# Optimization experiments

Measured on AMD Instinct MI355X. Metric: run time of the kernel, lower is better.

Reference implementation:

```python
import math
import jax, jax.numpy as jnp
import numpy as np

B, T, C, H = 4, 1024, 1024, 16


def setup_inputs() -> dict:
    key = jax.random.key(0)
    k1, k2, k3 = jax.random.split(key, 3)
    scale = 0.02
    return {
        "x": jax.random.normal(k1, (B, T, C), dtype=jnp.float32),
        "w_attn": jax.random.normal(k2, (C, 3 * C), dtype=jnp.float32) * scale,
        "b_attn": jnp.zeros((3 * C,), dtype=jnp.float32),
        "w_proj": jax.random.normal(k3, (C, C), dtype=jnp.float32) * scale,
        "b_proj": jnp.zeros((C,), dtype=jnp.float32),
    }


def reference(x, w_attn, b_attn, w_proj, b_proj):
    b, t, c = x.shape
    h = H
    d = c // h
    qkv = x @ w_attn + b_attn                      # [b, t, 3c]
    q, k, v = jnp.split(qkv, 3, axis=-1)
    # [b, h, t, d]
    q = q.reshape(b, t, h, d).transpose(0, 2, 1, 3)
    k = k.reshape(b, t, h, d).transpose(0, 2, 1, 3)
    v = v.reshape(b, t, h, d).transpose(0, 2, 1, 3)
    att = jnp.einsum("bhqd,bhkd->bhqk", q, k) * (1.0 / math.sqrt(d))
    causal = jnp.tril(jnp.ones((t, t), dtype=bool))
    att = jnp.where(causal[None, None], att, -jnp.inf)
    att = jax.nn.softmax(att, axis=-1)
    # dropout is identity in eval mode
    y = jnp.einsum("bhqk,bhkd->bhqd", att, v)      # [b, h, t, d]
    y = y.transpose(0, 2, 1, 3).reshape(b, t, c)
    return y @ w_proj + b_proj
```

## Files before the change

### kernel.cpp

```cpp
#include <hip/hip_runtime.h>

typedef __bf16 bf16;
typedef float f32x4 __attribute__((ext_vector_type(4)));
typedef bf16 bf16x4 __attribute__((ext_vector_type(4)));
typedef bf16 bf16x8 __attribute__((ext_vector_type(8)));

#define MFMA16(a, b, c) __builtin_amdgcn_mfma_f32_16x16x32_bf16((a), (b), (c), 0, 0, 0)

__device__ __forceinline__ f32x4 zero4() {
    f32x4 z; z[0] = 0.f; z[1] = 0.f; z[2] = 0.f; z[3] = 0.f; return z;
}
__device__ __forceinline__ void gl_lds16(const bf16* g, bf16* l) {
    __builtin_amdgcn_global_load_lds(
        (const __attribute__((address_space(1))) void*)g,
        (__attribute__((address_space(3))) void*)l, 16, 0, 0);
}

__global__ __launch_bounds__(256)
void prep_k(const float* __restrict__ x, bf16* __restrict__ xb,
            const float* __restrict__ w_attn, bf16* __restrict__ wT,
            const float* __restrict__ w_proj, bf16* __restrict__ wpT)
{
    __shared__ bf16 Ls[64][72];
    const int blk = blockIdx.x;
    const int tid = threadIdx.x;

    if (blk < 2048) {
        const int i = (blk * 256 + tid) * 8;
        const float4 a = *(const float4*)(x + i);
        const float4 b = *(const float4*)(x + i + 4);
        bf16x8 o;
        o[0] = (bf16)a.x; o[1] = (bf16)a.y; o[2] = (bf16)a.z; o[3] = (bf16)a.w;
        o[4] = (bf16)b.x; o[5] = (bf16)b.y; o[6] = (bf16)b.z; o[7] = (bf16)b.w;
        *(bf16x8*)(xb + i) = o;
        return;
    }
    const float* src;
    bf16* dst;
    int K, N, bx, by;
    if (blk < 2816) {
        const int r = blk - 2048;
        src = w_attn; dst = wT; K = 1024; N = 3072;
        bx = r % 48; by = r / 48;
    } else {
        const int r = blk - 2816;
        src = w_proj; dst = wpT; K = 1024; N = 1024;
        bx = r & 15; by = r >> 4;
    }
    const int k0 = by << 6;
    const int n0 = bx << 6;
    #pragma unroll
    for (int it = 0; it < 4; ++it) {
        const int lin = (it << 10) + (tid << 2);
        const int r = lin >> 6, c = lin & 63;
        const float4 v = *(const float4*)(src + (size_t)(k0 + r) * N + n0 + c);
        bf16x4 o; o[0] = (bf16)v.x; o[1] = (bf16)v.y; o[2] = (bf16)v.z; o[3] = (bf16)v.w;
        *(bf16x4*)&Ls[r][c] = o;
    }
    __syncthreads();
    #pragma unroll
    for (int it = 0; it < 2; ++it) {
        const int lin = (it << 11) + (tid << 3);
        const int nn = lin >> 6, kk = lin & 63;
        bf16x8 o;
        #pragma unroll
        for (int j = 0; j < 8; ++j) o[j] = Ls[kk + j][nn];
        *(bf16x8*)(dst + (size_t)(n0 + nn) * K + k0 + kk) = o;
    }
}

template <int MODE>
__global__ __launch_bounds__(256)
void gemm_bt(const bf16* __restrict__ A, const bf16* __restrict__ Bt,
             const float* __restrict__ bias,
             bf16* __restrict__ qw, bf16* __restrict__ kw, bf16* __restrict__ vw,
             float* __restrict__ outf, int M, int N, int K)
{
    constexpr int BK = 64;
    constexpr int BN = (MODE == 0) ? 128 : 64;
    constexpr int MF = (MODE == 0) ? 4 : 2;
    constexpr int NF = 4;
    constexpr int BI = (MODE == 0) ? 4 : 2;

    __shared__ __align__(16) bf16 smem[128 * BK + BN * BK];
    bf16* const As = smem;
    bf16* const Bs = smem + 128 * BK;

    const int tid  = threadIdx.x;
    const int lane = tid & 63;
    const int wid  = tid >> 6;
    const int l16  = lane & 15;
    const int g    = lane >> 4;
    const int wrb  = (MODE == 0) ? ((wid >> 1) << 6) : (wid << 5);
    const int wcb  = (MODE == 0) ? ((wid & 1) << 6) : 0;

    const int p   = blockIdx.x;
    const int xcd = p & 7;
    const int r   = p >> 3;
    int by, bx;
    if (MODE == 0) { by = ((xcd >> 1) << 3) + r / 12; bx = (xcd & 1) * 12 + r % 12; }
    else           { by = ((xcd >> 1) << 3) + (r >> 3); bx = ((xcd & 1) << 3) + (r & 7); }
    const int m0 = by << 7;
    const int n0 = bx * BN;

    const int srow = lane >> 3;
    const int sswz = ((lane & 7) ^ srow) << 3;
    const bf16* pa[4];
    const bf16* pb[BI];
    int dA[4], dB[BI];
    #pragma unroll
    for (int i = 0; i < 4; ++i) {
        const int R = (wid << 5) + (i << 3);
        pa[i] = A + (size_t)(m0 + R + srow) * K + sswz;
        dA[i] = R << 6;
    }
    #pragma unroll
    for (int i = 0; i < BI; ++i) {
        const int R = wid * (BN / 4) + (i << 3);
        pb[i] = Bt + (size_t)(n0 + R + srow) * K + sswz;
        dB[i] = R << 6;
    }

    int offA[2][MF], offB[2][NF];
    #pragma unroll
    for (int ks = 0; ks < 2; ++ks) {
        #pragma unroll
        for (int mf = 0; mf < MF; ++mf) {
            const int rr = wrb + (mf << 4) + l16;
            offA[ks][mf] = (rr << 6) + ((((ks << 2) + g) ^ (rr & 7)) << 3);
        }
        #pragma unroll
        for (int nf = 0; nf < NF; ++nf) {
            const int rr = wcb + (nf << 4) + l16;
            offB[ks][nf] = (rr << 6) + ((((ks << 2) + g) ^ (rr & 7)) << 3);
        }
    }

    f32x4 acc[MF][NF];
    #pragma unroll
    for (int i = 0; i < MF; ++i)
        #pragma unroll
        for (int j = 0; j < NF; ++j) acc[i][j] = zero4();

    const int nk = K >> 6;
    for (int kt = 0; kt < nk; ++kt) {
        const int k0 = kt << 6;
        __syncthreads();
        #pragma unroll
        for (int i = 0; i < 4; ++i)  gl_lds16(pa[i] + k0, As + dA[i]);
        #pragma unroll
        for (int i = 0; i < BI; ++i) gl_lds16(pb[i] + k0, Bs + dB[i]);
        __syncthreads();
        #pragma unroll
        for (int ks = 0; ks < 2; ++ks) {
            bf16x8 af[MF], bfr[NF];
            #pragma unroll
            for (int mf = 0; mf < MF; ++mf) af[mf] = *(const bf16x8*)&As[offA[ks][mf]];
            #pragma unroll
            for (int nf = 0; nf < NF; ++nf) bfr[nf] = *(const bf16x8*)&Bs[offB[ks][nf]];
            #pragma unroll
            for (int mf = 0; mf < MF; ++mf)
                #pragma unroll
                for (int nf = 0; nf < NF; ++nf)
                    acc[mf][nf] = MFMA16(af[mf], bfr[nf], acc[mf][nf]);
        }
    }
    __syncthreads();

    if (MODE == 0) {
        bf16* const Es = smem;
        const int bq  = m0 >> 10;
        const int tb  = m0 & 1023;
        const int hh0 = (n0 & 1023) >> 6;
        const bool isV = (n0 >= 2048);
        if (isV) {
            #pragma unroll
            for (int mf = 0; mf < MF; ++mf)
                #pragma unroll
                for (int nf = 0; nf < NF; ++nf) {
                    const int nn = wcb + (nf << 4) + l16;
                    const float bs = bias[n0 + nn];
                    bf16x4 pq;
                    #pragma unroll
                    for (int j = 0; j < 4; ++j) pq[j] = (bf16)(acc[mf][nf][j] + bs);
                    const int m = wrb + (mf << 4) + (g << 2);
                    const int pp = ((m >> 5) << 5) + (((m >> 2) & 3) << 3) + (((m >> 4) & 1) << 2);
                    *(bf16x4*)&Es[nn * 128 + pp] = pq;
                }
        } else {
            #pragma unroll
            for (int mf = 0; mf < MF; ++mf)
                #pragma unroll
                for (int nf = 0; nf < NF; ++nf) {
                    const int nn = wcb + (nf << 4) + l16;
                    const float bs = bias[n0 + nn];
                    #pragma unroll
                    for (int j = 0; j < 4; ++j) {
                        const int mm = wrb + (mf << 4) + (g << 2) + j;
                        Es[mm * 128 + nn] = (bf16)(acc[mf][nf][j] + bs);
                    }
                }
        }
        __syncthreads();
        #pragma unroll
        for (int it = 0; it < 8; ++it) {
            const int idx = (it << 8) + tid;
            const int row = idx >> 4, ch = idx & 15;
            const bf16x8 v = *(const bf16x8*)&Es[row * 128 + (ch << 3)];
            if (isV) {
                const int dd = row & 63, hh = hh0 + (row >> 6);
                *(bf16x8*)(vw + ((size_t)((bq << 4) + hh) << 16) + ((size_t)dd << 10)
                           + tb + (ch << 3)) = v;
            } else {
                const int t = tb + row;
                const int cc = ch << 3;
                const int hh = hh0 + (cc >> 6);
                bf16* const dst = (n0 < 1024) ? qw : kw;
                *(bf16x8*)(dst + ((size_t)((bq << 4) + hh) << 16) + ((size_t)t << 6)
                           + (cc & 63)) = v;
            }
        }
    } else {
        #pragma unroll
        for (int mf = 0; mf < MF; ++mf)
            #pragma unroll
            for (int nf = 0; nf < NF; ++nf) {
                const int ng = n0 + wcb + (nf << 4) + l16;
                const float bs = bias[ng];
                #pragma unroll
                for (int j = 0; j < 4; ++j) {
                    const int mg = m0 + wrb + (mf << 4) + (g << 2) + j;
                    outf[(size_t)mg * N + ng] = acc[mf][nf][j] + bs;
                }
            }
    }
}

__global__ __launch_bounds__(256)
void attn_k(const bf16* __restrict__ Qp, const bf16* __restrict__ Kp,
            const bf16* __restrict__ Vt, bf16* __restrict__ att)
{
    __shared__ __align__(16) bf16 Kl0[64 * 64], Kl1[64 * 64];
    __shared__ __align__(16) bf16 Vl0[64 * 64], Vl1[64 * 64];

    const int bh = blockIdx.x;
    const int bx = blockIdx.y;
    const int b  = bh >> 4, h = bh & 15;

    const int tid  = threadIdx.x;
    const int lane = tid & 63;
    const int wid  = tid >> 6;
    const int g    = lane >> 4;
    const int l16  = lane & 15;
    const int g8   = g << 3;

    const size_t hb = (size_t)bh << 16;
    const bf16* Qh = Qp + hb;
    const bf16* Kh = Kp + hb;
    const bf16* Vh = Vt + hb;

    const int srow = lane >> 3;
    const int sswz = ((lane & 7) ^ srow) << 3;
    const int kr0  = (wid << 4) + srow;
    const int kr1  = kr0 + 8;
    const int dst0 = (wid << 4) << 6;
    const int dst1 = ((wid << 4) + 8) << 6;

    int offKV[2][4];
    #pragma unroll
    for (int ks = 0; ks < 2; ++ks)
        #pragma unroll
        for (int cb = 0; cb < 4; ++cb) {
            const int r = (cb << 4) + l16;
            offKV[ks][cb] = (r << 6) + (((((ks << 2) + g)) ^ (r & 7)) << 3);
        }

    const float QSCALE = 0.125f * 1.44269504f;

    const int q1b = bx;
    const int q2b = 15 - bx;
    const int nkt = q2b;
    const int qloc = (wid << 4) + l16;

    const bf16* qp1 = Qh + ((size_t)((q1b << 6) + qloc) << 6) + g8;
    const bf16* qp2 = Qh + ((size_t)((q2b << 6) + qloc) << 6) + g8;
    bf16x8 q1f0 = *(const bf16x8*)qp1, q1f1 = *(const bf16x8*)(qp1 + 32);
    bf16x8 q2f0 = *(const bf16x8*)qp2, q2f1 = *(const bf16x8*)(qp2 + 32);
    #pragma unroll
    for (int e = 0; e < 8; ++e) {
        q1f0[e] = (bf16)(QSCALE * (float)q1f0[e]);
        q1f1[e] = (bf16)(QSCALE * (float)q1f1[e]);
        q2f0[e] = (bf16)(QSCALE * (float)q2f0[e]);
        q2f1[e] = (bf16)(QSCALE * (float)q2f1[e]);
    }

    f32x4 acc1[4], acc2[4];
    float m1 = -1e30f, l1 = 0.f, m2 = -1e30f, l2 = 0.f;
    #pragma unroll
    for (int i = 0; i < 4; ++i) { acc1[i] = zero4(); acc2[i] = zero4(); }

    gl_lds16(Kh + ((size_t)kr0 << 6) + sswz, Kl0 + dst0);
    gl_lds16(Kh + ((size_t)kr1 << 6) + sswz, Kl0 + dst1);
    gl_lds16(Vh + ((size_t)kr0 << 10) + sswz, Vl0 + dst0);
    gl_lds16(Vh + ((size_t)kr1 << 10) + sswz, Vl0 + dst1);
    __syncthreads();

    for (int kt = 0; kt <= nkt; ++kt) {
        const bool odd = kt & 1;
        if (kt < nkt) {
            const int kv1 = (kt + 1) << 6;
            bf16* Kn = odd ? Kl0 : Kl1;
            bf16* Vn = odd ? Vl0 : Vl1;
            gl_lds16(Kh + ((size_t)(kv1 + kr0) << 6) + sswz, Kn + dst0);
            gl_lds16(Kh + ((size_t)(kv1 + kr1) << 6) + sswz, Kn + dst1);
            gl_lds16(Vh + ((size_t)kr0 << 10) + kv1 + sswz, Vn + dst0);
            gl_lds16(Vh + ((size_t)kr1 << 10) + kv1 + sswz, Vn + dst1);
        }
        const bf16* Kc = odd ? Kl1 : Kl0;
        const bf16* Vc = odd ? Vl1 : Vl0;

        bf16x8 kf[2][4];
        #pragma unroll
        for (int ks = 0; ks < 2; ++ks)
            #pragma unroll
            for (int cb = 0; cb < 4; ++cb)
                kf[ks][cb] = *(const bf16x8*)&Kc[offKV[ks][cb]];

        {
            f32x4 sacc[4];
            #pragma unroll
            for (int cb = 0; cb < 4; ++cb) sacc[cb] = zero4();
            #pragma unroll
            for (int cb = 0; cb < 4; ++cb) sacc[cb] = MFMA16(kf[0][cb], q2f0, sacc[cb]);
            #pragma unroll
            for (int cb = 0; cb < 4; ++cb) sacc[cb] = MFMA16(kf[1][cb], q2f1, sacc[cb]);
            if (kt == q2b) {
                #pragma unroll
                for (int cb = 0; cb < 4; ++cb)
                    #pragma unroll
                    for (int j = 0; j < 4; ++j)
                        if (((cb << 4) + (g << 2) + j) > qloc) sacc[cb][j] = -1e30f;
            }
            float pm = sacc[0][0];
            #pragma unroll
            for (int cb = 0; cb < 4; ++cb)
                #pragma unroll
                for (int j = 0; j < 4; ++j) pm = fmaxf(pm, sacc[cb][j]);
            pm = fmaxf(pm, __shfl_xor(pm, 16));
            pm = fmaxf(pm, __shfl_xor(pm, 32));
            if (__any(pm > m2 + 8.f)) {
                const float mn = fmaxf(m2, pm);
                const float sc = __builtin_amdgcn_exp2f(m2 - mn);
                m2 = mn; l2 *= sc;
                #pragma unroll
                for (int db = 0; db < 4; ++db)
                    #pragma unroll
                    for (int j = 0; j < 4; ++j) acc2[db][j] *= sc;
            }
            float rsum = 0.f;
            #pragma unroll
            for (int cb = 0; cb < 4; ++cb)
                #pragma unroll
                for (int j = 0; j < 4; ++j) {
                    const float pv = __builtin_amdgcn_exp2f(sacc[cb][j] - m2);
                    sacc[cb][j] = pv;
                    rsum += pv;
                }
            rsum += __shfl_xor(rsum, 16);
            rsum += __shfl_xor(rsum, 32);
            l2 += rsum;
            bf16x8 pf0, pf1;
            #pragma unroll
            for (int i = 0; i < 8; ++i) {
                pf0[i] = (bf16)sacc[i >> 2][i & 3];
                pf1[i] = (bf16)sacc[2 + (i >> 2)][i & 3];
            }
            #pragma unroll
            for (int db = 0; db < 4; ++db) {
                const bf16x8 vf = *(const bf16x8*)&Vc[offKV[0][db]];
                acc2[db] = MFMA16(vf, pf0, acc2[db]);
            }
            #pragma unroll
            for (int db = 0; db < 4; ++db) {
                const bf16x8 vf = *(const bf16x8*)&Vc[offKV[1][db]];
                acc2[db] = MFMA16(vf, pf1, acc2[db]);
            }
        }

        if (kt <= q1b) {
            f32x4 sacc[4];
            #pragma unroll
            for (int cb = 0; cb < 4; ++cb) sacc[cb] = zero4();
            #pragma unroll
            for (int cb = 0; cb < 4; ++cb) sacc[cb] = MFMA16(kf[0][cb], q1f0, sacc[cb]);
            #pragma unroll
            for (int cb = 0; cb < 4; ++cb) sacc[cb] = MFMA16(kf[1][cb], q1f1, sacc[cb]);
            if (kt == q1b) {
                #pragma unroll
                for (int cb = 0; cb < 4; ++cb)
                    #pragma unroll
                    for (int j = 0; j < 4; ++j)
                        if (((cb << 4) + (g << 2) + j) > qloc) sacc[cb][j] = -1e30f;
            }
            float pm = sacc[0][0];
            #pragma unroll
            for (int cb = 0; cb < 4; ++cb)
                #pragma unroll
                for (int j = 0; j < 4; ++j) pm = fmaxf(pm, sacc[cb][j]);
            pm = fmaxf(pm, __shfl_xor(pm, 16));
            pm = fmaxf(pm, __shfl_xor(pm, 32));
            if (__any(pm > m1 + 8.f)) {
                const float mn = fmaxf(m1, pm);
                const float sc = __builtin_amdgcn_exp2f(m1 - mn);
                m1 = mn; l1 *= sc;
                #pragma unroll
                for (int db = 0; db < 4; ++db)
                    #pragma unroll
                    for (int j = 0; j < 4; ++j) acc1[db][j] *= sc;
            }
            float rsum = 0.f;
            #pragma unroll
            for (int cb = 0; cb < 4; ++cb)
                #pragma unroll
                for (int j = 0; j < 4; ++j) {
                    const float pv = __builtin_amdgcn_exp2f(sacc[cb][j] - m1);
                    sacc[cb][j] = pv;
                    rsum += pv;
                }
            rsum += __shfl_xor(rsum, 16);
            rsum += __shfl_xor(rsum, 32);
            l1 += rsum;
            bf16x8 pf0, pf1;
            #pragma unroll
            for (int i = 0; i < 8; ++i) {
                pf0[i] = (bf16)sacc[i >> 2][i & 3];
                pf1[i] = (bf16)sacc[2 + (i >> 2)][i & 3];
            }
            #pragma unroll
            for (int db = 0; db < 4; ++db) {
                const bf16x8 vf = *(const bf16x8*)&Vc[offKV[0][db]];
                acc1[db] = MFMA16(vf, pf0, acc1[db]);
            }
            #pragma unroll
            for (int db = 0; db < 4; ++db) {
                const bf16x8 vf = *(const bf16x8*)&Vc[offKV[1][db]];
                acc1[db] = MFMA16(vf, pf1, acc1[db]);
            }
        }
        __syncthreads();
    }

    {
        const float inv = 1.f / l2;
        const int t = (q2b << 6) + qloc;
        #pragma unroll
        for (int db = 0; db < 4; ++db) {
            bf16x4 o;
            #pragma unroll
            for (int j = 0; j < 4; ++j) o[j] = (bf16)(acc2[db][j] * inv);
            *(bf16x4*)(att + (((size_t)b << 10) + t) * 1024 + (h << 6) + (db << 4) + (g << 2)) = o;
        }
    }
    {
        const float inv = 1.f / l1;
        const int t = (q1b << 6) + qloc;
        #pragma unroll
        for (int db = 0; db < 4; ++db) {
            bf16x4 o;
            #pragma unroll
            for (int j = 0; j < 4; ++j) o[j] = (bf16)(acc1[db][j] * inv);
            *(bf16x4*)(att + (((size_t)b << 10) + t) * 1024 + (h << 6) + (db << 4) + (g << 2)) = o;
        }
    }
}

extern "C" void kernel_launch(void* const* d_in, const int* in_sizes, int n_in,
                              void* d_out, int out_size, void* d_ws, size_t ws_size,
                              hipStream_t stream)
{
    const float* x      = (const float*)d_in[0];
    const float* w_attn = (const float*)d_in[1];
    const float* b_attn = (const float*)d_in[2];
    const float* w_proj = (const float*)d_in[3];
    const float* b_proj = (const float*)d_in[4];
    float* out = (float*)d_out;

    bf16* xb  = (bf16*)d_ws;
    bf16* wT  = xb  + (size_t)4096 * 1024;
    bf16* wpT = wT  + (size_t)3072 * 1024;
    bf16* qw  = wpT + (size_t)1024 * 1024;
    bf16* kw  = qw  + (size_t)64 * 1024 * 64;
    bf16* vw  = kw  + (size_t)64 * 1024 * 64;
    bf16* aw  = vw  + (size_t)64 * 1024 * 64;

    prep_k<<<3072, 256, 0, stream>>>(x, xb, w_attn, wT, w_proj, wpT);

    gemm_bt<0><<<768, 256, 0, stream>>>(xb, wT, b_attn, qw, kw, vw,
                                        nullptr, 4096, 3072, 1024);
    attn_k<<<dim3(64, 8), 256, 0, stream>>>(qw, kw, vw, aw);
    gemm_bt<1><<<512, 256, 0, stream>>>(aw, wpT, b_proj, nullptr, nullptr, nullptr,
                                        out, 4096, 1024, 1024);
}
```

Before: 95.99 us.

## Triple-buffer GEMM K-loop with async LDS loads and vmcnt-based waits

```diff
diff --git a/kernel.cpp b/kernel.cpp
--- a/kernel.cpp
+++ b/kernel.cpp
@@ -74,17 +74,21 @@
 void gemm_bt(const bf16* __restrict__ A, const bf16* __restrict__ Bt,
              const float* __restrict__ bias,
              bf16* __restrict__ qw, bf16* __restrict__ kw, bf16* __restrict__ vw,
-             float* __restrict__ outf, int M, int N, int K)
+             float* __restrict__ outf)
 {
-    constexpr int BK = 64;
+    constexpr int BK = 32;
     constexpr int BN = (MODE == 0) ? 128 : 64;
+    constexpr int K  = 1024;
+    constexpr int N  = (MODE == 0) ? 3072 : 1024;
     constexpr int MF = (MODE == 0) ? 4 : 2;
     constexpr int NF = 4;
-    constexpr int BI = (MODE == 0) ? 4 : 2;
-
-    __shared__ __align__(16) bf16 smem[128 * BK + BN * BK];
-    bf16* const As = smem;
-    bf16* const Bs = smem + 128 * BK;
+    constexpr int AE = 128 * BK;
+    constexpr int BE = BN * BK;
+    constexpr int nk = K / BK;
+
+    __shared__ __align__(16) bf16 smem[3 * (AE + BE)];
+    bf16* const Asb = smem;
+    bf16* const Bsb = smem + 3 * AE;
 
     const int tid  = threadIdx.x;
     const int lane = tid & 63;
@@ -103,37 +107,29 @@
     const int m0 = by << 7;
     const int n0 = bx * BN;
 
-    const int srow = lane >> 3;
-    const int sswz = ((lane & 7) ^ srow) << 3;
-    const bf16* pa[4];
-    const bf16* pb[BI];
-    int dA[4], dB[BI];
-    #pragma unroll
-    for (int i = 0; i < 4; ++i) {
-        const int R = (wid << 5) + (i << 3);
-        pa[i] = A + (size_t)(m0 + R + srow) * K + sswz;
-        dA[i] = R << 6;
-    }
-    #pragma unroll
-    for (int i = 0; i < BI; ++i) {
-        const int R = wid * (BN / 4) + (i << 3);
-        pb[i] = Bt + (size_t)(n0 + R + srow) * K + sswz;
-        dB[i] = R << 6;
-    }
-
-    int offA[2][MF], offB[2][NF];
-    #pragma unroll
-    for (int ks = 0; ks < 2; ++ks) {
-        #pragma unroll
-        for (int mf = 0; mf < MF; ++mf) {
-            const int rr = wrb + (mf << 4) + l16;
-            offA[ks][mf] = (rr << 6) + ((((ks << 2) + g) ^ (rr & 7)) << 3);
-        }
-        #pragma unroll
-        for (int nf = 0; nf < NF; ++nf) {
-            const int rr = wcb + (nf << 4) + l16;
-            offB[ks][nf] = (rr << 6) + ((((ks << 2) + g) ^ (rr & 7)) << 3);
-        }
+    const int srow = lane >> 2;
+    const int schk = lane & 3;
+    const int rA0 = (wid << 5) + srow;
+    const int rA1 = rA0 + 16;
+    const int rB0 = wid * (BN / 4) + srow;
+    const int rB1 = rB0 + 16;
+    const bf16* const pa0 = A  + (size_t)(m0 + rA0) * K + ((schk ^ ((rA0 >> 1) & 3)) << 3);
+    const bf16* const pa1 = A  + (size_t)(m0 + rA1) * K + ((schk ^ ((rA1 >> 1) & 3)) << 3);
+    const bf16* const pb0 = Bt + (size_t)(n0 + rB0) * K + ((schk ^ ((rB0 >> 1) & 3)) << 3);
+    const bf16* const pb1 = Bt + (size_t)(n0 + rB1) * K + ((schk ^ ((rB1 >> 1) & 3)) << 3);
+    const int dA0 = (wid << 5) * BK, dA1 = dA0 + 16 * BK;
+    const int dB0 = (wid * (BN / 4)) * BK, dB1 = dB0 + 16 * BK;
+
+    int offA[MF], offB[NF];
+    #pragma unroll
+    for (int mf = 0; mf < MF; ++mf) {
+        const int rr = wrb + (mf << 4) + l16;
+        offA[mf] = rr * BK + ((g ^ ((rr >> 1) & 3)) << 3);
+    }
+    #pragma unroll
+    for (int nf = 0; nf < NF; ++nf) {
+        const int rr = wcb + (nf << 4) + l16;
+        offB[nf] = rr * BK + ((g ^ ((rr >> 1) & 3)) << 3);
     }
 
     f32x4 acc[MF][NF];
@@ -142,28 +138,42 @@
         #pragma unroll
         for (int j = 0; j < NF; ++j) acc[i][j] = zero4();
 
-    const int nk = K >> 6;
+    auto issue = [&](int t, int s) {
+        bf16* const ab = Asb + s * AE;
+        bf16* const bb = Bsb + s * BE;
+        gl_lds16(pa0 + t * BK, ab + dA0);
+        gl_lds16(pa1 + t * BK, ab + dA1);
+        gl_lds16(pb0 + t * BK, bb + dB0);
+        if constexpr (MODE == 0) gl_lds16(pb1 + t * BK, bb + dB1);
+    };
+
+    issue(0, 0);
+    issue(1, 1);
+
+    #pragma unroll
     for (int kt = 0; kt < nk; ++kt) {
-        const int k0 = kt << 6;
-        __syncthreads();
-        #pragma unroll
-        for (int i = 0; i < 4; ++i)  gl_lds16(pa[i] + k0, As + dA[i]);
-        #pragma unroll
-        for (int i = 0; i < BI; ++i) gl_lds16(pb[i] + k0, Bs + dB[i]);
-        __syncthreads();
-        #pragma unroll
-        for (int ks = 0; ks < 2; ++ks) {
-            bf16x8 af[MF], bfr[NF];
-            #pragma unroll
-            for (int mf = 0; mf < MF; ++mf) af[mf] = *(const bf16x8*)&As[offA[ks][mf]];
-            #pragma unroll
-            for (int nf = 0; nf < NF; ++nf) bfr[nf] = *(const bf16x8*)&Bs[offB[ks][nf]];
-            #pragma unroll
-            for (int mf = 0; mf < MF; ++mf)
-                #pragma unroll
-                for (int nf = 0; nf < NF; ++nf)
-                    acc[mf][nf] = MFMA16(af[mf], bfr[nf], acc[mf][nf]);
-        }
+        if (kt == nk - 1) {
+            asm volatile("s_waitcnt vmcnt(0)" ::: "memory");
+        } else {
+            if constexpr (MODE == 0) asm volatile("s_waitcnt vmcnt(4)" ::: "memory");
+            else                     asm volatile("s_waitcnt vmcnt(3)" ::: "memory");
+        }
+        __builtin_amdgcn_s_barrier();
+        if (kt + 2 < nk) issue(kt + 2, (kt + 2) % 3);
+        const bf16* const ac = Asb + (kt % 3) * AE;
+        const bf16* const bc = Bsb + (kt % 3) * BE;
+        bf16x8 af[MF], bfr[NF];
+        #pragma unroll
+        for (int mf = 0; mf < MF; ++mf) af[mf] = *(const bf16x8*)&ac[offA[mf]];
+        #pragma unroll
+        for (int nf = 0; nf < NF; ++nf) bfr[nf] = *(const bf16x8*)&bc[offB[nf]];
+        __builtin_amdgcn_s_setprio(1);
+        #pragma unroll
+        for (int mf = 0; mf < MF; ++mf)
+            #pragma unroll
+            for (int nf = 0; nf < NF; ++nf)
+                acc[mf][nf] = MFMA16(af[mf], bfr[nf], acc[mf][nf]);
+        __builtin_amdgcn_s_setprio(0);
     }
     __syncthreads();
 
@@ -495,9 +505,7 @@
 
     prep_k<<<3072, 256, 0, stream>>>(x, xb, w_attn, wT, w_proj, wpT);
 
-    gemm_bt<0><<<768, 256, 0, stream>>>(xb, wT, b_attn, qw, kw, vw,
-                                        nullptr, 4096, 3072, 1024);
+    gemm_bt<0><<<768, 256, 0, stream>>>(xb, wT, b_attn, qw, kw, vw, nullptr);
     attn_k<<<dim3(64, 8), 256, 0, stream>>>(qw, kw, vw, aw);
-    gemm_bt<1><<<512, 256, 0, stream>>>(aw, wpT, b_proj, nullptr, nullptr, nullptr,
-                                        out, 4096, 1024, 1024);
+    gemm_bt<1><<<512, 256, 0, stream>>>(aw, wpT, b_proj, nullptr, nullptr, nullptr, out);
 }
```

Measured after the change: 84.87 us. 11.6% less time.
